# Performance work log

Hardware: AMD Instinct MI355X
Metric: run time of the kernel (lower is better)

Reference implementation:

```python
import jax, jax.numpy as jnp
import numpy as np

TAU = 2.0
ALPHA = 4.0  # spikingjelly surrogate.Sigmoid default
NUM_HEADS = 8


def lif(x, v_th):
    # Multi-step LIF over leading time axis T. v_reset=0, hard reset, tau=2.
    # Forward: Heaviside spike; backward: sigmoid surrogate via straight-through.
    def step(v, xt):
        v = v + (xt - v) / TAU
        hard = (v >= v_th).astype(xt.dtype)
        soft = jax.nn.sigmoid(ALPHA * (v - v_th))
        spike = soft + jax.lax.stop_gradient(hard - soft)
        v = v * (1.0 - jax.lax.stop_gradient(hard))  # detach_reset hard reset to 0
        return v, spike
    _, out = jax.lax.scan(step, jnp.zeros_like(x[0]), x)
    return out


def conv_bn_lif(x, w, scale, bias, v_th=1.0):
    # 1x1 conv (no bias) + folded eval-mode BatchNorm + LIF.
    # x: [T,B,C,H,W], w: [Cout,Cin], scale/bias: [Cout]
    y = jnp.einsum('tbchw,dc->tbdhw', x, w)
    y = y * scale[:, None, None] + bias[:, None, None]
    return lif(y, v_th)


def setup_inputs() -> dict:
    key = jax.random.key(0)
    ks = jax.random.split(key, 14)
    T, B, C, H, W = 4, 32, 384, 14, 14
    x = jax.random.normal(ks[0], (T, B, C, H, W), dtype=jnp.float32)
    def conv_params(k):
        k1, k2, k3 = jax.random.split(k, 3)
        w = jax.random.normal(k1, (C, C), dtype=jnp.float32) * (1.0 / np.sqrt(C))
        scale = jax.random.uniform(k2, (C,), dtype=jnp.float32, minval=0.5, maxval=1.5)
        bias = jax.random.normal(k3, (C,), dtype=jnp.float32) * 0.1
        return w, scale, bias
    wq, sq, bq = conv_params(ks[1])
    wk, sk, bk = conv_params(ks[2])
    wv, sv, bv = conv_params(ks[3])
    wp, sp, bp = conv_params(ks[4])
    return {"x": x, "wq": wq, "sq": sq, "bq": bq, "wk": wk, "sk": sk, "bk": bk,
            "wv": wv, "sv": sv, "bv": bv, "wp": wp, "sp": sp, "bp": bp}


def reference(x, wq, sq, bq, wk, sk, bk, wv, sv, bv, wp, sp, bp):
    T, B, C, H, W = x.shape
    h = NUM_HEADS
    d = C // h
    N = H * W
    # QKV: conv+BN+LIF -> binary spikes [T,B,C,H,W]
    qs = conv_bn_lif(x, wq, sq, bq)
    ks_ = conv_bn_lif(x, wk, sk, bk)
    vs = conv_bn_lif(x, wv, sv, bv)
    # [T,B,C,H,W] -> [T,B,h,d,N] -> [T,B,h,N,d]
    def to_heads(t):
        return t.reshape(T, B, h, d, N).transpose(0, 1, 2, 4, 3)
    q, k, v = to_heads(qs), to_heads(ks_), to_heads(vs)
    attn = jnp.einsum('tbhnd,tbhmd->tbhnm', q, k)
    out = jnp.einsum('tbhnm,tbhmd->tbhnd', attn, v) * 0.125
    out = lif(out, 0.5)  # attn_lif v_threshold=0.5
    # [T,B,h,N,d] -> [T,B,h,d,N] -> [T,B,C,H,W]
    out = out.transpose(0, 1, 2, 4, 3).reshape(T, B, C, H, W)
    out = conv_bn_lif(out, wp, sp, bp)
    return out
```

## Files before the change

kernel.cpp:

```cpp
#include <hip/hip_runtime.h>


#define T_ 4
#define B_ 32
#define C_ 384
#define N_ 196
#define NH_ 8
#define D_ 48
#define TB_ (T_ * B_)
#define CN_ ((size_t)C_ * N_)
#define BCN4_ (B_ * C_ * (N_ / 4))
#define TBCN_ ((size_t)T_ * B_ * C_ * N_)
typedef unsigned long long u64;

__global__ __launch_bounds__(256) void gemm_f32(
    const float* __restrict__ X, const float* __restrict__ W0,
    const float* __restrict__ W1, const float* __restrict__ W2,
    float* __restrict__ P)
{
  const int g = blockIdx.z;
  const float* __restrict__ W = (g == 0) ? W0 : (g == 1) ? W1 : W2;
  const int co0 = blockIdx.y * 128;
  const int j0 = blockIdx.x * 128;
  __shared__ float As[16][128];
  __shared__ float Bs[16][128];
  const int tid = threadIdx.x;
  const int tx = tid & 15, ty = tid >> 4;

  const int bcol = (tid & 31) * 4;
  const int bk = tid >> 5;
  const int bj = j0 + bcol;
  const int btb = bj / N_;
  const float* xb = X + (size_t)btb * CN_ + (bj - btb * N_);
  const int arow = tid >> 1;
  const int ac8 = (tid & 1) * 8;
  const float* wrow0 = W + (size_t)(co0 + arow) * C_ + ac8;

  float4 pa0 = *(const float4*)(wrow0);
  float4 pa1 = *(const float4*)(wrow0 + 4);
  float4 pb0 = *(const float4*)(xb + (size_t)bk * N_);
  float4 pb1 = *(const float4*)(xb + (size_t)(bk + 8) * N_);

  float acc[8][8] = {};
  for (int c0 = 0; c0 < C_; c0 += 16) {
    __syncthreads();
    As[ac8 + 0][arow] = pa0.x; As[ac8 + 1][arow] = pa0.y;
    As[ac8 + 2][arow] = pa0.z; As[ac8 + 3][arow] = pa0.w;
    As[ac8 + 4][arow] = pa1.x; As[ac8 + 5][arow] = pa1.y;
    As[ac8 + 6][arow] = pa1.z; As[ac8 + 7][arow] = pa1.w;
    *(float4*)&Bs[bk][bcol] = pb0;
    *(float4*)&Bs[bk + 8][bcol] = pb1;
    __syncthreads();
    if (c0 + 16 < C_) {
      pa0 = *(const float4*)(wrow0 + c0 + 16);
      pa1 = *(const float4*)(wrow0 + c0 + 20);
      pb0 = *(const float4*)(xb + (size_t)(c0 + 16 + bk) * N_);
      pb1 = *(const float4*)(xb + (size_t)(c0 + 24 + bk) * N_);
    }
#pragma unroll
    for (int k = 0; k < 16; ++k) {
      float a[8], b[8];
      *(float4*)&a[0] = *(const float4*)&As[k][ty * 4];
      *(float4*)&a[4] = *(const float4*)&As[k][64 + ty * 4];
      *(float4*)&b[0] = *(const float4*)&Bs[k][tx * 4];
      *(float4*)&b[4] = *(const float4*)&Bs[k][64 + tx * 4];
#pragma unroll
      for (int i = 0; i < 8; ++i)
#pragma unroll
        for (int j = 0; j < 8; ++j)
          acc[i][j] = fmaf(a[i], b[j], acc[i][j]);
    }
  }
#pragma unroll
  for (int cg = 0; cg < 2; ++cg) {
    const int jj = j0 + cg * 64 + tx * 4;
    const int tb = jj / N_;
    float* pb = P + (size_t)(g * TB_ + tb) * CN_ + (jj - tb * N_);
#pragma unroll
    for (int rg = 0; rg < 2; ++rg) {
#pragma unroll
      for (int i = 0; i < 4; ++i) {
        const int r = rg * 4 + i;
        const int co = co0 + rg * 64 + ty * 4 + i;
        *(float4*)&pb[(size_t)co * N_] = make_float4(
            acc[r][cg * 4 + 0], acc[r][cg * 4 + 1],
            acc[r][cg * 4 + 2], acc[r][cg * 4 + 3]);
      }
    }
  }
}

__global__ __launch_bounds__(256) void lif4(
    const float* __restrict__ In, float* __restrict__ Out,
    const float* __restrict__ s0, const float* __restrict__ b0, float vth)
{
  const long u = (long)blockIdx.x * 256 + threadIdx.x;
  if (u >= BCN4_) return;
  const long r = u;
  const int c = (int)((r / (N_ / 4)) % C_);
  const bool has_bn = (s0 != nullptr);
  const float sc = has_bn ? s0[c] : 1.0f;
  const float bi = has_bn ? b0[c] : 0.0f;
  const float4* In4 = (const float4*)In;
  float4* Out4 = (float4*)Out;
  float v[4] = {0.f, 0.f, 0.f, 0.f};
#pragma unroll
  for (int t = 0; t < T_; ++t) {
    const long idx = (long)t * BCN4_ + r;
    const float4 y4 = In4[idx];
    float y[4] = {y4.x, y4.y, y4.z, y4.w};
    float o[4];
#pragma unroll
    for (int e = 0; e < 4; ++e) {
      const float yb = has_bn ? __fadd_rn(__fmul_rn(y[e], sc), bi) : y[e];
      v[e] = __fadd_rn(v[e], __fmul_rn(__fsub_rn(yb, v[e]), 0.5f));
      const bool fire = (v[e] >= vth);
      o[e] = fire ? 1.0f : 0.0f;
      v[e] = fire ? 0.0f : v[e];
    }
    Out4[idx] = make_float4(o[0], o[1], o[2], o[3]);
  }
}

__global__ __launch_bounds__(256) void k_mask(
    const float* __restrict__ P, u64* __restrict__ MSK,
    const float* __restrict__ sq, const float* __restrict__ bq,
    const float* __restrict__ sk, const float* __restrict__ bk,
    const float* __restrict__ sv, const float* __restrict__ bv)
{
  const int wave = threadIdx.x >> 6, lane = threadIdx.x & 63;
  const int task = blockIdx.x * 4 + wave;
  const int j = task % D_;
  int r = task / D_;
  const int b = r & 31; r >>= 5;
  const int h = r & 7;  r >>= 3;
  const int g = r;
  const int c = h * D_ + j;
  const float sc = (g == 0 ? sq : g == 1 ? sk : sv)[c];
  const float bi = (g == 0 ? bq : g == 1 ? bk : bv)[c];
  const float* base = P + (size_t)g * TB_ * CN_ + (size_t)b * CN_ + (size_t)c * N_;

  float y[4][T_];
  bool act[4];
#pragma unroll
  for (int w = 0; w < 4; ++w) {
    const int m = w * 64 + lane;
    act[w] = (m < N_);
    const int mc = act[w] ? m : (N_ - 1);
#pragma unroll
    for (int t = 0; t < T_; ++t)
      y[w][t] = base[(size_t)t * B_ * CN_ + mc];
  }
  u64* mb = MSK + ((size_t)(h * 32 + b) * 3 + g) * (T_ * D_ * 4) + j * 4;
  float v[4] = {0.f, 0.f, 0.f, 0.f};
#pragma unroll
  for (int t = 0; t < T_; ++t) {
#pragma unroll
    for (int w = 0; w < 4; ++w) {
      const float yb = __fadd_rn(__fmul_rn(y[w][t], sc), bi);
      v[w] = __fadd_rn(v[w], __fmul_rn(__fsub_rn(yb, v[w]), 0.5f));
      const bool fire = (v[w] >= 1.0f);
      if (fire) v[w] = 0.f;
      const u64 bl = __ballot(fire && act[w]);
      if (lane == 0) mb[(size_t)t * (D_ * 4) + w] = bl;
    }
  }
}

__global__ __launch_bounds__(1024) void k_attn(
    const u64* __restrict__ MSK, float* __restrict__ O)
{
  const int h = blockIdx.x;
  const int b = blockIdx.y;
  __shared__ u64 msk[3][T_][D_][4];
  __shared__ u64 qT[T_][208];
  __shared__ u64 Gp[T_][8][D_];
  const int tid = threadIdx.x;
  const int wave = tid >> 6, lane = tid & 63;

  {
    const u64* ms = MSK + (size_t)(h * 32 + b) * 2304;
    u64* mf = &msk[0][0][0][0];
    for (int off = tid; off < 2304; off += 1024) mf[off] = ms[off];
  }
  __syncthreads();

  {
    const int t = wave >> 2, w = wave & 3;
    const int n = w * 64 + lane;
    u64 qr = 0ull;
#pragma unroll 8
    for (int j = 0; j < D_; ++j)
      qr |= ((msk[0][t][j][w] >> lane) & 1ull) << j;
    if (n < N_) qT[t][n] = qr;
  }
  for (int task = wave; task < T_ * D_; task += 16) {
    const int t = task / D_, d = task - (task / D_) * D_;
    const bool ja = (lane < D_);
    const int j = ja ? lane : (D_ - 1);
    const u64* kj = msk[1][t][j];
    const u64* vd = msk[2][t][d];
    const int gi = __popcll(kj[0] & vd[0]) + __popcll(kj[1] & vd[1]) +
                   __popcll(kj[2] & vd[2]) + __popcll(kj[3] & vd[3]);
#pragma unroll
    for (int p = 0; p < 8; ++p) {
      const u64 bl = __ballot(ja && ((gi >> p) & 1));
      if (lane == 0) Gp[t][p][d] = bl;
    }
  }
  __syncthreads();

  const int u = tid;
  if (u < 4 * N_) {
    const int dq = u / N_;
    const int n = u - dq * N_;
    const int d0 = dq * 12;
    float vmem[12];
#pragma unroll
    for (int i = 0; i < 12; ++i) vmem[i] = 0.f;
    for (int t = 0; t < T_; ++t) {
      const u64 qr = qT[t][n];
      float* ob = O + ((size_t)(t * B_ + b) * C_ + h * D_ + d0) * N_ + n;
#pragma unroll
      for (int i = 0; i < 12; ++i) {
        int acc = 0;
#pragma unroll
        for (int p = 0; p < 8; ++p)
          acc += __popcll(qr & Gp[t][p][d0 + i]) << p;
        const float y = __int2float_rn(acc) * 0.125f;
        vmem[i] = __fadd_rn(vmem[i], __fmul_rn(__fsub_rn(y, vmem[i]), 0.5f));
        const bool fire = (vmem[i] >= 0.5f);
        ob[(size_t)i * N_] = fire ? 1.0f : 0.0f;
        if (fire) vmem[i] = 0.f;
      }
    }
  }
}

extern "C" void kernel_launch(void* const* d_in, const int* in_sizes, int n_in,
                              void* d_out, int out_size, void* d_ws, size_t ws_size,
                              hipStream_t stream) {
  const float* x  = (const float*)d_in[0];
  const float* wq = (const float*)d_in[1];
  const float* sq = (const float*)d_in[2];
  const float* bq = (const float*)d_in[3];
  const float* wk = (const float*)d_in[4];
  const float* sk = (const float*)d_in[5];
  const float* bk = (const float*)d_in[6];
  const float* wv = (const float*)d_in[7];
  const float* sv = (const float*)d_in[8];
  const float* bv = (const float*)d_in[9];
  const float* wp = (const float*)d_in[10];
  const float* sp = (const float*)d_in[11];
  const float* bp = (const float*)d_in[12];
  float* out = (float*)d_out;

  float* P = (float*)d_ws;
  float* O = P + 3 * TBCN_;
  u64* MSK = (u64*)(P + 4 * TBCN_);
  float* P2 = P;

  gemm_f32<<<dim3(196, 3, 3), 256, 0, stream>>>(x, wq, wk, wv, P);
  k_mask<<<dim3(9216), 256, 0, stream>>>(P, MSK, sq, bq, sk, bk, sv, bv);
  k_attn<<<dim3(NH_, B_), 1024, 0, stream>>>(MSK, O);
  gemm_f32<<<dim3(196, 3, 1), 256, 0, stream>>>(O, wp, wp, wp, P2);
  lif4<<<dim3((BCN4_ + 255) / 256), 256, 0, stream>>>(P2, out, sp, bp, 1.0f);
}
```

Baseline: 512.4 us.

## Fuse BN+LIF into GEMM epilogue with time-interleaved tiles and byte spike output

The GEMM tile now maps its 128 columns to 32 spatial positions across all 4 timesteps, so the LIF recurrence can run in the epilogue straight from registers. Spikes are written as bytes for QKV and as floats for the projection output. The separate k_mask and lif4 kernels are removed, and bitmask packing moves into the attention kernel's load phase. This removes the float round-trips of the intermediate pre-activations, but the epilogue stores become scalar and strided, and the B-tile smem stores lose vectorization.

```diff
diff --git a/kernel.cpp b/kernel.cpp
--- a/kernel.cpp
+++ b/kernel.cpp
@@ -9,29 +9,37 @@
 #define D_ 48
 #define TB_ (T_ * B_)
 #define CN_ ((size_t)C_ * N_)
-#define BCN4_ (B_ * C_ * (N_ / 4))
 #define TBCN_ ((size_t)T_ * B_ * C_ * N_)
 typedef unsigned long long u64;
 
-__global__ __launch_bounds__(256) void gemm_f32(
+template <bool BYTE_OUT>
+__global__ __launch_bounds__(256) void gemm_lif(
     const float* __restrict__ X, const float* __restrict__ W0,
     const float* __restrict__ W1, const float* __restrict__ W2,
-    float* __restrict__ P)
+    const float* __restrict__ s0, const float* __restrict__ b0_,
+    const float* __restrict__ s1, const float* __restrict__ b1_,
+    const float* __restrict__ s2, const float* __restrict__ b2_,
+    unsigned char* __restrict__ SB, float* __restrict__ FO)
 {
   const int g = blockIdx.z;
-  const float* __restrict__ W = (g == 0) ? W0 : (g == 1) ? W1 : W2;
+  const float* __restrict__ W  = (g == 0) ? W0 : (g == 1) ? W1 : W2;
+  const float* __restrict__ SC = (g == 0) ? s0 : (g == 1) ? s1 : s2;
+  const float* __restrict__ BI = (g == 0) ? b0_ : (g == 1) ? b1_ : b2_;
   const int co0 = blockIdx.y * 128;
-  const int j0 = blockIdx.x * 128;
+  const int p0 = blockIdx.x * 32;
   __shared__ float As[16][128];
   __shared__ float Bs[16][128];
   const int tid = threadIdx.x;
   const int tx = tid & 15, ty = tid >> 4;
 
-  const int bcol = (tid & 31) * 4;
+  const int ct = tid & 31;
+  const int bt = ct & 3;
+  const int uq = ct >> 2;
   const int bk = tid >> 5;
-  const int bj = j0 + bcol;
-  const int btb = bj / N_;
-  const float* xb = X + (size_t)btb * CN_ + (bj - btb * N_);
+  const int pq = p0 + uq * 4;
+  const int bb = pq / N_;
+  const int nn = pq - bb * N_;
+  const float* xb = X + (size_t)(bt * B_ + bb) * CN_ + nn;
   const int arow = tid >> 1;
   const int ac8 = (tid & 1) * 8;
   const float* wrow0 = W + (size_t)(co0 + arow) * C_ + ac8;
@@ -48,8 +56,14 @@
     As[ac8 + 2][arow] = pa0.z; As[ac8 + 3][arow] = pa0.w;
     As[ac8 + 4][arow] = pa1.x; As[ac8 + 5][arow] = pa1.y;
     As[ac8 + 6][arow] = pa1.z; As[ac8 + 7][arow] = pa1.w;
-    *(float4*)&Bs[bk][bcol] = pb0;
-    *(float4*)&Bs[bk + 8][bcol] = pb1;
+    Bs[bk][16 * uq + 0 + bt] = pb0.x;
+    Bs[bk][16 * uq + 4 + bt] = pb0.y;
+    Bs[bk][16 * uq + 8 + bt] = pb0.z;
+    Bs[bk][16 * uq + 12 + bt] = pb0.w;
+    Bs[bk + 8][16 * uq + 0 + bt] = pb1.x;
+    Bs[bk + 8][16 * uq + 4 + bt] = pb1.y;
+    Bs[bk + 8][16 * uq + 8 + bt] = pb1.z;
+    Bs[bk + 8][16 * uq + 12 + bt] = pb1.w;
     __syncthreads();
     if (c0 + 16 < C_) {
       pa0 = *(const float4*)(wrow0 + c0 + 16);
@@ -71,104 +85,44 @@
           acc[i][j] = fmaf(a[i], b[j], acc[i][j]);
     }
   }
-#pragma unroll
-  for (int cg = 0; cg < 2; ++cg) {
-    const int jj = j0 + cg * 64 + tx * 4;
-    const int tb = jj / N_;
-    float* pb = P + (size_t)(g * TB_ + tb) * CN_ + (jj - tb * N_);
-#pragma unroll
-    for (int rg = 0; rg < 2; ++rg) {
-#pragma unroll
-      for (int i = 0; i < 4; ++i) {
-        const int r = rg * 4 + i;
-        const int co = co0 + rg * 64 + ty * 4 + i;
-        *(float4*)&pb[(size_t)co * N_] = make_float4(
-            acc[r][cg * 4 + 0], acc[r][cg * 4 + 1],
-            acc[r][cg * 4 + 2], acc[r][cg * 4 + 3]);
+  int bArr[2], nArr[2];
+#pragma unroll
+  for (int ug = 0; ug < 2; ++ug) {
+    const int p = p0 + ug * 16 + tx;
+    bArr[ug] = p / N_;
+    nArr[ug] = p - bArr[ug] * N_;
+  }
+#pragma unroll
+  for (int rg = 0; rg < 2; ++rg) {
+#pragma unroll
+    for (int i = 0; i < 4; ++i) {
+      const int r = rg * 4 + i;
+      const int co = co0 + rg * 64 + ty * 4 + i;
+      const float sc = SC[co];
+      const float bi = BI[co];
+#pragma unroll
+      for (int ug = 0; ug < 2; ++ug) {
+        const int b2 = bArr[ug], n2 = nArr[ug];
+        float v = 0.f;
+#pragma unroll
+        for (int t = 0; t < T_; ++t) {
+          const float y = acc[r][ug * 4 + t];
+          const float yb = __fadd_rn(__fmul_rn(y, sc), bi);
+          v = __fadd_rn(v, __fmul_rn(__fsub_rn(yb, v), 0.5f));
+          const bool fire = (v >= 1.0f);
+          const size_t off =
+              ((size_t)((g * T_ + t) * B_ + b2) * C_ + co) * N_ + n2;
+          if (BYTE_OUT) SB[off] = fire ? (unsigned char)1 : (unsigned char)0;
+          else          FO[off] = fire ? 1.0f : 0.0f;
+          if (fire) v = 0.f;
+        }
       }
     }
   }
 }
 
-__global__ __launch_bounds__(256) void lif4(
-    const float* __restrict__ In, float* __restrict__ Out,
-    const float* __restrict__ s0, const float* __restrict__ b0, float vth)
-{
-  const long u = (long)blockIdx.x * 256 + threadIdx.x;
-  if (u >= BCN4_) return;
-  const long r = u;
-  const int c = (int)((r / (N_ / 4)) % C_);
-  const bool has_bn = (s0 != nullptr);
-  const float sc = has_bn ? s0[c] : 1.0f;
-  const float bi = has_bn ? b0[c] : 0.0f;
-  const float4* In4 = (const float4*)In;
-  float4* Out4 = (float4*)Out;
-  float v[4] = {0.f, 0.f, 0.f, 0.f};
-#pragma unroll
-  for (int t = 0; t < T_; ++t) {
-    const long idx = (long)t * BCN4_ + r;
-    const float4 y4 = In4[idx];
-    float y[4] = {y4.x, y4.y, y4.z, y4.w};
-    float o[4];
-#pragma unroll
-    for (int e = 0; e < 4; ++e) {
-      const float yb = has_bn ? __fadd_rn(__fmul_rn(y[e], sc), bi) : y[e];
-      v[e] = __fadd_rn(v[e], __fmul_rn(__fsub_rn(yb, v[e]), 0.5f));
-      const bool fire = (v[e] >= vth);
-      o[e] = fire ? 1.0f : 0.0f;
-      v[e] = fire ? 0.0f : v[e];
-    }
-    Out4[idx] = make_float4(o[0], o[1], o[2], o[3]);
-  }
-}
-
-__global__ __launch_bounds__(256) void k_mask(
-    const float* __restrict__ P, u64* __restrict__ MSK,
-    const float* __restrict__ sq, const float* __restrict__ bq,
-    const float* __restrict__ sk, const float* __restrict__ bk,
-    const float* __restrict__ sv, const float* __restrict__ bv)
-{
-  const int wave = threadIdx.x >> 6, lane = threadIdx.x & 63;
-  const int task = blockIdx.x * 4 + wave;
-  const int j = task % D_;
-  int r = task / D_;
-  const int b = r & 31; r >>= 5;
-  const int h = r & 7;  r >>= 3;
-  const int g = r;
-  const int c = h * D_ + j;
-  const float sc = (g == 0 ? sq : g == 1 ? sk : sv)[c];
-  const float bi = (g == 0 ? bq : g == 1 ? bk : bv)[c];
-  const float* base = P + (size_t)g * TB_ * CN_ + (size_t)b * CN_ + (size_t)c * N_;
-
-  float y[4][T_];
-  bool act[4];
-#pragma unroll
-  for (int w = 0; w < 4; ++w) {
-    const int m = w * 64 + lane;
-    act[w] = (m < N_);
-    const int mc = act[w] ? m : (N_ - 1);
-#pragma unroll
-    for (int t = 0; t < T_; ++t)
-      y[w][t] = base[(size_t)t * B_ * CN_ + mc];
-  }
-  u64* mb = MSK + ((size_t)(h * 32 + b) * 3 + g) * (T_ * D_ * 4) + j * 4;
-  float v[4] = {0.f, 0.f, 0.f, 0.f};
-#pragma unroll
-  for (int t = 0; t < T_; ++t) {
-#pragma unroll
-    for (int w = 0; w < 4; ++w) {
-      const float yb = __fadd_rn(__fmul_rn(y[w][t], sc), bi);
-      v[w] = __fadd_rn(v[w], __fmul_rn(__fsub_rn(yb, v[w]), 0.5f));
-      const bool fire = (v[w] >= 1.0f);
-      if (fire) v[w] = 0.f;
-      const u64 bl = __ballot(fire && act[w]);
-      if (lane == 0) mb[(size_t)t * (D_ * 4) + w] = bl;
-    }
-  }
-}
-
 __global__ __launch_bounds__(1024) void k_attn(
-    const u64* __restrict__ MSK, float* __restrict__ O)
+    const unsigned char* __restrict__ S, float* __restrict__ O)
 {
   const int h = blockIdx.x;
   const int b = blockIdx.y;
@@ -178,10 +132,28 @@
   const int tid = threadIdx.x;
   const int wave = tid >> 6, lane = tid & 63;
 
-  {
-    const u64* ms = MSK + (size_t)(h * 32 + b) * 2304;
-    u64* mf = &msk[0][0][0][0];
-    for (int off = tid; off < 2304; off += 1024) mf[off] = ms[off];
+  for (int task = wave; task < 3 * D_; task += 16) {
+    const int g = task / D_;
+    const int j = task - g * D_;
+    const int c = h * D_ + j;
+    unsigned char yb[T_][4];
+    bool act[4];
+#pragma unroll
+    for (int w = 0; w < 4; ++w) {
+      const int m = w * 64 + lane;
+      act[w] = (m < N_);
+      const int mc = act[w] ? m : (N_ - 1);
+#pragma unroll
+      for (int t = 0; t < T_; ++t)
+        yb[t][w] = S[((size_t)((g * T_ + t) * B_ + b) * C_ + c) * N_ + mc];
+    }
+#pragma unroll
+    for (int t = 0; t < T_; ++t)
+#pragma unroll
+      for (int w = 0; w < 4; ++w) {
+        const u64 bl = __ballot(act[w] && (yb[t][w] != 0));
+        if (lane == 0) msk[g][t][j][w] = bl;
+      }
   }
   __syncthreads();
 
@@ -255,14 +227,12 @@
   const float* bp = (const float*)d_in[12];
   float* out = (float*)d_out;
 
-  float* P = (float*)d_ws;
-  float* O = P + 3 * TBCN_;
-  u64* MSK = (u64*)(P + 4 * TBCN_);
-  float* P2 = P;
-
-  gemm_f32<<<dim3(196, 3, 3), 256, 0, stream>>>(x, wq, wk, wv, P);
-  k_mask<<<dim3(9216), 256, 0, stream>>>(P, MSK, sq, bq, sk, bk, sv, bv);
-  k_attn<<<dim3(NH_, B_), 1024, 0, stream>>>(MSK, O);
-  gemm_f32<<<dim3(196, 3, 1), 256, 0, stream>>>(O, wp, wp, wp, P2);
-  lif4<<<dim3((BCN4_ + 255) / 256), 256, 0, stream>>>(P2, out, sp, bp, 1.0f);
+  unsigned char* S = (unsigned char*)d_ws;
+  float* O = (float*)(S + 3 * TBCN_);
+
+  gemm_lif<true><<<dim3(196, 3, 3), 256, 0, stream>>>(
+      x, wq, wk, wv, sq, bq, sk, bk, sv, bv, S, nullptr);
+  k_attn<<<dim3(NH_, B_), 1024, 0, stream>>>(S, O);
+  gemm_lif<false><<<dim3(196, 3, 1), 256, 0, stream>>>(
+      O, wp, wp, wp, sp, bp, sp, bp, sp, bp, nullptr, out);
 }
```

Result: slower. 628.3 us (+22.6%).
